# Performance work log

Hardware: AMD Instinct MI355X
Metric: run time of the kernel (lower is better)

## Reference

```python
import jax, jax.numpy as jnp
import numpy as np

B, T, S, F = 4, 256, 128, 256
H, V = 512, 1024


def setup_inputs() -> dict:
    key = jax.random.key(0)
    ks = jax.random.split(key, 4)
    return {
        "source_encodings": jax.random.normal(ks[0], (B, T, F), dtype=jnp.float32),
        "target_encodings": jax.random.normal(ks[1], (B, S, F), dtype=jnp.float32),
        "W1": jax.random.normal(ks[2], (2 * F, H), dtype=jnp.float32) * (1.0 / np.sqrt(2 * F)),
        "b1": jnp.zeros((H,), dtype=jnp.float32),
        "W2": jax.random.normal(ks[3], (H, V), dtype=jnp.float32) * (1.0 / np.sqrt(H)),
        "b2": jnp.zeros((V,), dtype=jnp.float32),
    }


def reference(source_encodings, target_encodings, W1, b1, W2, b2):
    # source: [B,T,F] -> [B,T,S,F]; target: [B,S,F] -> [B,T,S,F]
    b, t, f = source_encodings.shape
    s = target_encodings.shape[1]
    src = jnp.broadcast_to(source_encodings[:, :, None, :], (b, t, s, f))
    tgt = jnp.broadcast_to(target_encodings[:, None, :, :], (b, t, s, f))
    x = jnp.concatenate([src, tgt], axis=-1)  # [B,T,S,2F]
    h = jax.nn.relu(jnp.einsum("btsf,fh->btsh", x, W1) + b1)
    logits = jnp.einsum("btsh,hv->btsv", h, W2) + b2
    # eval-mode path applies log_softmax over the vocab axis
    return jax.nn.log_softmax(logits, axis=-1)
```

## Files before the change

### kernel.cpp

```cpp
#include <hip/hip_runtime.h>
#include <hip/hip_bf16.h>

#define Bb 4
#define Tt 256
#define Ss 128
#define Ff 256
#define Hh 512
#define Vv 1024

typedef __attribute__((ext_vector_type(8))) short bf16x8;
typedef __attribute__((ext_vector_type(4))) float f32x4;

__global__ __launch_bounds__(256) void precompute_kernel(
    const float* __restrict__ src, const float* __restrict__ tgt,
    const float* __restrict__ W1, const float* __restrict__ b1,
    float* __restrict__ hs, float* __restrict__ ht)
{
    __shared__ float rows[8][Ff];
    const int blk = blockIdx.x;
    const bool is_hs = blk < (Bb * Tt / 8);
    const int row0 = is_hs ? blk * 8 : (blk - Bb * Tt / 8) * 8;
    const float* in = (is_hs ? src : tgt) + row0 * Ff;
    const float* w  = is_hs ? W1 : (W1 + Ff * Hh);
    float* out      = is_hs ? hs : ht;
    const int t = threadIdx.x;

    for (int i = t; i < 8 * Ff; i += 256) rows[i >> 8][i & (Ff - 1)] = in[i];
    __syncthreads();

    float acc0[8], acc1[8];
#pragma unroll
    for (int r = 0; r < 8; r++) { acc0[r] = 0.f; acc1[r] = 0.f; }

    for (int k = 0; k < Ff; k++) {
        const float w0 = w[k * Hh + t];
        const float w1 = w[k * Hh + t + 256];
#pragma unroll
        for (int r = 0; r < 8; r++) {
            const float x = rows[r][k];
            acc0[r] = fmaf(x, w0, acc0[r]);
            acc1[r] = fmaf(x, w1, acc1[r]);
        }
    }
    const float bias0 = is_hs ? b1[t]       : 0.f;
    const float bias1 = is_hs ? b1[t + 256] : 0.f;
#pragma unroll
    for (int r = 0; r < 8; r++) {
        out[(row0 + r) * Hh + t]       = acc0[r] + bias0;
        out[(row0 + r) * Hh + t + 256] = acc1[r] + bias1;
    }
}

__global__ __launch_bounds__(256) void w2t_kernel(
    const float* __restrict__ W2, __hip_bfloat16* __restrict__ W2T)
{
    const int idx = blockIdx.x * 256 + threadIdx.x;
    const int v = idx >> 9;
    const int h = idx & (Hh - 1);
    W2T[idx] = __float2bfloat16(W2[h * Vv + v]);
}

__global__ __launch_bounds__(512, 2) void joint_main_kernel(
    const float* __restrict__ hs, const float* __restrict__ ht,
    const __hip_bfloat16* __restrict__ W2T, const float* __restrict__ b2,
    float* __restrict__ out)
{
    __shared__ __hip_bfloat16 Abuf[2][64][32];
    __shared__ float redmax[64][8];
    __shared__ float redsum[64][8];

    const int blk  = blockIdx.x;
    const int bt   = blk >> 1;
    const int s0   = (blk & 1) * 64;
    const int b    = bt >> 8;
    const int tid  = threadIdx.x;
    const int w    = tid >> 6;
    const int lane = tid & 63;
    const int quad = lane >> 4;
    const int l15  = lane & 15;

    const float* hsrow  = hs + bt * Hh;
    const float* htbase = ht + (b * Ss + s0) * Hh;

    const int ar  = tid >> 3;
    const int akc = (tid & 7) * 4;
    const float* hs_a = hsrow + akc;
    const float* ht_a = htbase + ar * Hh + akc;

    const __hip_bfloat16* bbase = W2T + (w * 128 + l15) * Hh + quad * 8;

    f32x4 acc[4][8];
#pragma unroll
    for (int rt = 0; rt < 4; rt++)
#pragma unroll
        for (int ct = 0; ct < 8; ct++) {
            f32x4 z = {0.f, 0.f, 0.f, 0.f};
            acc[rt][ct] = z;
        }

    bf16x8 bfrag[2][8];

#define STAGE_A(ki, buf) do {                                              \
        const float4 xa = *(const float4*)(hs_a + (ki) * 32);              \
        const float4 xb = *(const float4*)(ht_a + (ki) * 32);              \
        union { __hip_bfloat16 h[4]; uint2 u; } pk;                        \
        pk.h[0] = __float2bfloat16(fmaxf(xa.x + xb.x, 0.f));               \
        pk.h[1] = __float2bfloat16(fmaxf(xa.y + xb.y, 0.f));               \
        pk.h[2] = __float2bfloat16(fmaxf(xa.z + xb.z, 0.f));               \
        pk.h[3] = __float2bfloat16(fmaxf(xa.w + xb.w, 0.f));               \
        *(uint2*)&Abuf[buf][ar][akc] = pk.u;                               \
    } while (0)

#define LOAD_B(ki, buf) do {                                               \
        _Pragma("unroll")                                                  \
        for (int ct = 0; ct < 8; ct++)                                     \
            bfrag[buf][ct] =                                               \
                *(const bf16x8*)(bbase + ct * 16 * Hh + (ki) * 32);        \
    } while (0)

    STAGE_A(0, 0);
    LOAD_B(0, 0);
    __syncthreads();

#pragma unroll
    for (int ki = 0; ki < 16; ki++) {
        const int cur = ki & 1, nxt = cur ^ 1;
        if (ki < 15) {
            LOAD_B(ki + 1, nxt);
            STAGE_A(ki + 1, nxt);
        }
        bf16x8 afrag[4];
#pragma unroll
        for (int rt = 0; rt < 4; rt++)
            afrag[rt] = *(const bf16x8*)&Abuf[cur][rt * 16 + l15][quad * 8];
#pragma unroll
        for (int rt = 0; rt < 4; rt++)
#pragma unroll
            for (int ct = 0; ct < 8; ct++)
                acc[rt][ct] = __builtin_amdgcn_mfma_f32_16x16x32_bf16(
                    afrag[rt], bfrag[cur][ct], acc[rt][ct], 0, 0, 0);
        __syncthreads();
    }
#undef STAGE_A
#undef LOAD_B

    float b2v[8];
#pragma unroll
    for (int ct = 0; ct < 8; ct++) b2v[ct] = b2[w * 128 + ct * 16 + l15];
#pragma unroll
    for (int rt = 0; rt < 4; rt++)
#pragma unroll
        for (int ct = 0; ct < 8; ct++) {
            acc[rt][ct].x += b2v[ct]; acc[rt][ct].y += b2v[ct];
            acc[rt][ct].z += b2v[ct]; acc[rt][ct].w += b2v[ct];
        }

    float mrow[4][4];
#pragma unroll
    for (int rt = 0; rt < 4; rt++)
#pragma unroll
        for (int r = 0; r < 4; r++) {
            float m = acc[rt][0][r];
#pragma unroll
            for (int ct = 1; ct < 8; ct++) m = fmaxf(m, acc[rt][ct][r]);
            mrow[rt][r] = m;
        }
#pragma unroll
    for (int off = 8; off >= 1; off >>= 1)
#pragma unroll
        for (int rt = 0; rt < 4; rt++)
#pragma unroll
            for (int r = 0; r < 4; r++)
                mrow[rt][r] = fmaxf(mrow[rt][r], __shfl_xor(mrow[rt][r], off, 64));

    if (l15 == 0) {
#pragma unroll
        for (int rt = 0; rt < 4; rt++)
#pragma unroll
            for (int r = 0; r < 4; r++)
                redmax[rt * 16 + quad * 4 + r][w] = mrow[rt][r];
    }
    __syncthreads();

    float gmax[4][4];
#pragma unroll
    for (int rt = 0; rt < 4; rt++)
#pragma unroll
        for (int r = 0; r < 4; r++) {
            const int row = rt * 16 + quad * 4 + r;
            float m = redmax[row][0];
#pragma unroll
            for (int wv = 1; wv < 8; wv++) m = fmaxf(m, redmax[row][wv]);
            gmax[rt][r] = m;
        }

    float srow[4][4];
#pragma unroll
    for (int rt = 0; rt < 4; rt++)
#pragma unroll
        for (int r = 0; r < 4; r++) {
            float s = 0.f;
#pragma unroll
            for (int ct = 0; ct < 8; ct++)
                s += __expf(acc[rt][ct][r] - gmax[rt][r]);
            srow[rt][r] = s;
        }
#pragma unroll
    for (int off = 8; off >= 1; off >>= 1)
#pragma unroll
        for (int rt = 0; rt < 4; rt++)
#pragma unroll
            for (int r = 0; r < 4; r++)
                srow[rt][r] += __shfl_xor(srow[rt][r], off, 64);

    if (l15 == 0) {
#pragma unroll
        for (int rt = 0; rt < 4; rt++)
#pragma unroll
            for (int r = 0; r < 4; r++)
                redsum[rt * 16 + quad * 4 + r][w] = srow[rt][r];
    }
    __syncthreads();

#pragma unroll
    for (int rt = 0; rt < 4; rt++)
#pragma unroll
        for (int r = 0; r < 4; r++) {
            const int row = rt * 16 + quad * 4 + r;
            float s = redsum[row][0];
#pragma unroll
            for (int wv = 1; wv < 8; wv++) s += redsum[row][wv];
            const float lse = gmax[rt][r] + __logf(s);
            const int mg = bt * Ss + s0 + row;
            float* orow = out + (size_t)mg * Vv + w * 128 + l15;
#pragma unroll
            for (int ct = 0; ct < 8; ct++)
                orow[ct * 16] = acc[rt][ct][r] - lse;
        }
}

extern "C" void kernel_launch(void* const* d_in, const int* in_sizes, int n_in,
                              void* d_out, int out_size, void* d_ws, size_t ws_size,
                              hipStream_t stream)
{
    const float* src = (const float*)d_in[0];
    const float* tgt = (const float*)d_in[1];
    const float* W1  = (const float*)d_in[2];
    const float* b1  = (const float*)d_in[3];
    const float* W2  = (const float*)d_in[4];
    const float* b2  = (const float*)d_in[5];
    float* outp = (float*)d_out;

    char* ws = (char*)d_ws;
    float* hs = (float*)ws;
    float* ht = (float*)(ws + (size_t)(Bb * Tt * Hh) * 4);
    __hip_bfloat16* W2T =
        (__hip_bfloat16*)(ws + (size_t)(Bb * Tt * Hh + Bb * Ss * Hh) * 4);

    hipLaunchKernelGGL(precompute_kernel, dim3((Bb * Tt + Bb * Ss) / 8), dim3(256),
                       0, stream, src, tgt, W1, b1, hs, ht);
    hipLaunchKernelGGL(w2t_kernel, dim3(Vv * Hh / 256), dim3(256),
                       0, stream, W2, W2T);
    hipLaunchKernelGGL(joint_main_kernel, dim3(Bb * Tt * Ss / 64), dim3(512),
                       0, stream, hs, ht, W2T, b2, outp);
}
```

Measured before the change: 858.8 us.

## Stage full A tile in LDS once and drop per-step barriers; nontemporal output stores

The main kernel now builds the entire 64x512 bf16 activation tile (relu(hs+ht)) in shared memory up front, with padded rows, instead of double-buffering 32-wide K slices. This removes the __syncthreads from every K step, leaving only the register-level B prefetch in the loop. Output stores use nontemporal hints to avoid polluting cache with the large logits write. The cost is much more LDS per block (about 66KB), which may limit how many blocks fit per CU.

```diff
diff --git a/kernel.cpp b/kernel.cpp
--- a/kernel.cpp
+++ b/kernel.cpp
@@ -60,12 +60,14 @@
     W2T[idx] = __float2bfloat16(W2[h * Vv + v]);
 }
 
+#define APAD 520
+
 __global__ __launch_bounds__(512, 2) void joint_main_kernel(
     const float* __restrict__ hs, const float* __restrict__ ht,
     const __hip_bfloat16* __restrict__ W2T, const float* __restrict__ b2,
     float* __restrict__ out)
 {
-    __shared__ __hip_bfloat16 Abuf[2][64][32];
+    __shared__ __hip_bfloat16 Abuf[64][APAD];
     __shared__ float redmax[64][8];
     __shared__ float redsum[64][8];
 
@@ -82,35 +84,9 @@
     const float* hsrow  = hs + bt * Hh;
     const float* htbase = ht + (b * Ss + s0) * Hh;
 
-    const int ar  = tid >> 3;
-    const int akc = (tid & 7) * 4;
-    const float* hs_a = hsrow + akc;
-    const float* ht_a = htbase + ar * Hh + akc;
-
     const __hip_bfloat16* bbase = W2T + (w * 128 + l15) * Hh + quad * 8;
 
-    f32x4 acc[4][8];
-#pragma unroll
-    for (int rt = 0; rt < 4; rt++)
-#pragma unroll
-        for (int ct = 0; ct < 8; ct++) {
-            f32x4 z = {0.f, 0.f, 0.f, 0.f};
-            acc[rt][ct] = z;
-        }
-
     bf16x8 bfrag[2][8];
-
-#define STAGE_A(ki, buf) do {                                              \
-        const float4 xa = *(const float4*)(hs_a + (ki) * 32);              \
-        const float4 xb = *(const float4*)(ht_a + (ki) * 32);              \
-        union { __hip_bfloat16 h[4]; uint2 u; } pk;                        \
-        pk.h[0] = __float2bfloat16(fmaxf(xa.x + xb.x, 0.f));               \
-        pk.h[1] = __float2bfloat16(fmaxf(xa.y + xb.y, 0.f));               \
-        pk.h[2] = __float2bfloat16(fmaxf(xa.z + xb.z, 0.f));               \
-        pk.h[3] = __float2bfloat16(fmaxf(xa.w + xb.w, 0.f));               \
-        *(uint2*)&Abuf[buf][ar][akc] = pk.u;                               \
-    } while (0)
-
 #define LOAD_B(ki, buf) do {                                               \
         _Pragma("unroll")                                                  \
         for (int ct = 0; ct < 8; ct++)                                     \
@@ -118,30 +94,56 @@
                 *(const bf16x8*)(bbase + ct * 16 * Hh + (ki) * 32);        \
     } while (0)
 
-    STAGE_A(0, 0);
     LOAD_B(0, 0);
-    __syncthreads();
+
+#pragma unroll
+    for (int it = 0; it < 8; ++it) {
+        const int idx = it * 512 + tid;
+        const int r   = idx >> 6;
+        const int c   = (idx & 63) * 8;
+        const float* hp = hsrow + c;
+        const float* tp = htbase + r * Hh + c;
+        const float4 a0 = *(const float4*)(hp);
+        const float4 a1 = *(const float4*)(hp + 4);
+        const float4 b0 = *(const float4*)(tp);
+        const float4 b1 = *(const float4*)(tp + 4);
+        union { __hip_bfloat16 h[8]; bf16x8 v; } pk;
+        pk.h[0] = __float2bfloat16(fmaxf(a0.x + b0.x, 0.f));
+        pk.h[1] = __float2bfloat16(fmaxf(a0.y + b0.y, 0.f));
+        pk.h[2] = __float2bfloat16(fmaxf(a0.z + b0.z, 0.f));
+        pk.h[3] = __float2bfloat16(fmaxf(a0.w + b0.w, 0.f));
+        pk.h[4] = __float2bfloat16(fmaxf(a1.x + b1.x, 0.f));
+        pk.h[5] = __float2bfloat16(fmaxf(a1.y + b1.y, 0.f));
+        pk.h[6] = __float2bfloat16(fmaxf(a1.z + b1.z, 0.f));
+        pk.h[7] = __float2bfloat16(fmaxf(a1.w + b1.w, 0.f));
+        *(bf16x8*)&Abuf[r][c] = pk.v;
+    }
+    __syncthreads();
+
+    f32x4 acc[4][8];
+#pragma unroll
+    for (int rt = 0; rt < 4; rt++)
+#pragma unroll
+        for (int ct = 0; ct < 8; ct++) {
+            f32x4 z = {0.f, 0.f, 0.f, 0.f};
+            acc[rt][ct] = z;
+        }
 
 #pragma unroll
     for (int ki = 0; ki < 16; ki++) {
-        const int cur = ki & 1, nxt = cur ^ 1;
-        if (ki < 15) {
-            LOAD_B(ki + 1, nxt);
-            STAGE_A(ki + 1, nxt);
-        }
+        const int cur = ki & 1;
         bf16x8 afrag[4];
 #pragma unroll
         for (int rt = 0; rt < 4; rt++)
-            afrag[rt] = *(const bf16x8*)&Abuf[cur][rt * 16 + l15][quad * 8];
+            afrag[rt] = *(const bf16x8*)&Abuf[rt * 16 + l15][ki * 32 + quad * 8];
+        if (ki < 15) LOAD_B(ki + 1, cur ^ 1);
 #pragma unroll
         for (int rt = 0; rt < 4; rt++)
 #pragma unroll
             for (int ct = 0; ct < 8; ct++)
                 acc[rt][ct] = __builtin_amdgcn_mfma_f32_16x16x32_bf16(
                     afrag[rt], bfrag[cur][ct], acc[rt][ct], 0, 0, 0);
-        __syncthreads();
-    }
-#undef STAGE_A
+    }
 #undef LOAD_B
 
     float b2v[8];
@@ -235,7 +237,7 @@
             float* orow = out + (size_t)mg * Vv + w * 128 + l15;
 #pragma unroll
             for (int ct = 0; ct < 8; ct++)
-                orow[ct * 16] = acc[rt][ct][r] - lse;
+                __builtin_nontemporal_store(acc[rt][ct][r] - lse, &orow[ct * 16]);
         }
 }
 
```

Result: faster. 834.9 us (-2.8%).
